# Kernel tuning notes

Measured on AMD Instinct MI355X. Metric: run time of the kernel, lower is better.

## Reference

```python
import jax, jax.numpy as jnp
import numpy as np

L = 8      # n_layers
D = 512    # msa_dim
P = 128    # pair_dim
H = 8      # n_heads
HD = D // H  # head_dim = 64
B = 2
NS = 4
S = 384


def setup_inputs() -> dict:
    key = jax.random.key(0)
    ks = jax.random.split(key, 24)
    def rn(k, shape, s=0.02):
        return jax.random.normal(k, shape, dtype=jnp.float32) * s
    return {
        "msa_repr": jax.random.normal(ks[0], (B, NS, S, D), dtype=jnp.float32),
        "pair_repr": jax.random.normal(ks[1], (B, S, S, P), dtype=jnp.float32),
        # per-layer IPA params, stacked along layer axis
        "Wq": rn(ks[2], (L, D, D)), "bq": jnp.zeros((L, D), jnp.float32),
        "Wk": rn(ks[3], (L, D, D)), "bk": jnp.zeros((L, D), jnp.float32),
        "Wv": rn(ks[4], (L, D, D)), "bv": jnp.zeros((L, D), jnp.float32),
        "Wpb": rn(ks[5], (L, P, H)), "bpb": jnp.zeros((L, H), jnp.float32),
        "Wo": rn(ks[6], (L, D, D)), "bo": jnp.zeros((L, D), jnp.float32),
        # shared backbone_update MLP (applied after every layer)
        "Wb1": rn(ks[7], (D, D)), "bb1": jnp.zeros((D,), jnp.float32),
        "Wb2": rn(ks[8], (D, 6)), "bb2": jnp.zeros((6,), jnp.float32),
        # confidence head
        "Wc1": rn(ks[9], (D, D // 2)), "bc1": jnp.zeros((D // 2,), jnp.float32),
        "Wc2": rn(ks[10], (D // 2, 1)), "bc2": jnp.zeros((1,), jnp.float32),
    }


def reference(msa_repr, pair_repr, Wq, bq, Wk, bk, Wv, bv, Wpb, bpb, Wo, bo,
              Wb1, bb1, Wb2, bb2, Wc1, bc1, Wc2, bc2):
    Bd, n_seqs, Sd, Dm = msa_repr.shape
    x0 = msa_repr[:, 0]                      # [B,S,D] target sequence repr
    coords0 = jnp.zeros((Bd, Sd, 3), msa_repr.dtype)
    inv_sqrt_hd = jnp.asarray(1.0 / np.sqrt(HD), msa_repr.dtype)

    def layer(carry, p):
        x, coords = carry
        wq, bq_, wk, bk_, wv, bv_, wpb, bpb_, wo, bo_ = p
        q = (x @ wq + bq_).reshape(Bd, Sd, H, HD)
        k = (x @ wk + bk_).reshape(Bd, Sd, H, HD)
        v = (x @ wv + bv_).reshape(Bd, Sd, H, HD)
        scores = jnp.einsum('bihd,bjhd->bhij', q, k) * inv_sqrt_hd
        bias = jnp.einsum('bijp,ph->bhij', pair_repr, wpb) + bpb_[None, :, None, None]
        attn = jax.nn.softmax(scores + bias, axis=-1)   # dropout=0 (eval)
        out = jnp.einsum('bhij,bjhd->bihd', attn, v).reshape(Bd, Sd, Dm)
        x = x + out @ wo + bo_                          # residual
        upd = jax.nn.relu(x @ Wb1 + bb1) @ Wb2 + bb2    # [B,S,6]
        coords = coords + upd[..., :3]                  # translation only
        return (x, coords), None

    (x, coords), _ = jax.lax.scan(layer, (x0, coords0),
                                  (Wq, bq, Wk, bk, Wv, bv, Wpb, bpb, Wo, bo))
    confidence = jax.nn.sigmoid(jax.nn.relu(x @ Wc1 + bc1) @ Wc2 + bc2)[..., 0]
    return coords, confidence
```

## Files before the change

### kernel.cpp

```cpp
#include <hip/hip_runtime.h>
#include <math.h>

#define L 8
#define D 512
#define DD (D*D)
#define P 128
#define H 8
#define HD 64
#define B 2
#define NS 4
#define S 384
#define BS (B*S)
#define XN (BS*D)
#define SS ((size_t)S*S)
#define BHSS ((size_t)B*H*S*S)
#define NSLAB 32

typedef short bf16x8 __attribute__((ext_vector_type(8)));
typedef float f32x4 __attribute__((ext_vector_type(4)));

__device__ __forceinline__ unsigned short f2b(float f) {
    unsigned u = __float_as_uint(f);
    unsigned r = (u + 0x7FFF + ((u >> 16) & 1)) >> 16;
    return (unsigned short)r;
}
__device__ __forceinline__ float b2f(unsigned short u) {
    return __uint_as_float(((unsigned)u) << 16);
}

__global__ __launch_bounds__(256) void k_init(const float* __restrict__ msa,
                                              float* __restrict__ x,
                                              unsigned short* __restrict__ xb,
                                              float* __restrict__ part) {
    int idx = blockIdx.x * 256 + threadIdx.x;
    if (idx < XN) {
        int b = idx / (S * D);
        int rem = idx - b * (S * D);
        float v = msa[(size_t)b * NS * S * D + rem];
        x[idx] = v;
        xb[idx] = f2b(v);
    }
    if (idx < NSLAB * BS * 3) part[idx] = 0.f;
}

__global__ __launch_bounds__(256) void k_prep(const float* __restrict__ Wq,
        const float* __restrict__ Wk, const float* __restrict__ Wv,
        const float* __restrict__ Wo, const float* __restrict__ Wb1,
        const float* __restrict__ Wc1, unsigned short* __restrict__ wt) {
    __shared__ float ts[64][65];
    const int z = blockIdx.z;
    const float* src; int N = 512;
    if (z < 8)       src = Wq + (size_t)z * DD;
    else if (z < 16) src = Wk + (size_t)(z - 8) * DD;
    else if (z < 24) src = Wv + (size_t)(z - 16) * DD;
    else if (z < 32) src = Wo + (size_t)(z - 24) * DD;
    else if (z == 32) src = Wb1;
    else { src = Wc1; N = 256; }
    unsigned short* dst = wt + (size_t)z * DD;

    const int n0 = blockIdx.x * 64, k0 = blockIdx.y * 64;
    if (n0 >= N) return;
    const int t = threadIdx.x;
    #pragma unroll
    for (int m = 0; m < 16; m++) {
        int f = t + m * 256;
        int r = f >> 6, c = f & 63;
        ts[r][c] = src[(size_t)(k0 + r) * N + n0 + c];
    }
    __syncthreads();
    #pragma unroll
    for (int m = 0; m < 4; m++) {
        int o4 = t + m * 256;
        int nr = o4 >> 4, k4 = o4 & 15;
        ushort4 pk;
        pk.x = f2b(ts[k4 * 4 + 0][nr]);
        pk.y = f2b(ts[k4 * 4 + 1][nr]);
        pk.z = f2b(ts[k4 * 4 + 2][nr]);
        pk.w = f2b(ts[k4 * 4 + 3][nr]);
        *(ushort4*)&dst[(size_t)(n0 + nr) * 512 + k0 + k4 * 4] = pk;
    }
}

__global__ __launch_bounds__(256) void k_biasm(const float* __restrict__ pair,
        const float* __restrict__ Wpb, const float* __restrict__ bpb,
        unsigned short* __restrict__ bias) {
    __shared__ unsigned short Ws[64][136];
    __shared__ unsigned short Ps[64][136];
    const int t = threadIdx.x;
    const int lane = t & 63, w = t >> 6;
    const int jt = blockIdx.x, i = blockIdx.y, b = blockIdx.z;

    #pragma unroll
    for (int m = 0; m < 8; m++) {
        int f = (t + m * 256) * 4;
        float4 wv = *(const float4*)&Wpb[f];
        int l = f >> 10, rem = f & 1023;
        int k = rem >> 3, h = rem & 7;
        int lh = (l << 3) | h;
        Ws[lh + 0][k] = f2b(wv.x);
        Ws[lh + 1][k] = f2b(wv.y);
        Ws[lh + 2][k] = f2b(wv.z);
        Ws[lh + 3][k] = f2b(wv.w);
    }
    const float* prow = pair + (((size_t)b * S + i) * S + jt * 64) * P;
    #pragma unroll
    for (int m = 0; m < 8; m++) {
        int f = (t + m * 256) * 4;
        int r = f >> 7, c = f & 127;
        float4 pv = *(const float4*)&prow[f];
        ushort4 u;
        u.x = f2b(pv.x); u.y = f2b(pv.y); u.z = f2b(pv.z); u.w = f2b(pv.w);
        *(ushort4*)&Ps[r][c] = u;
    }
    __syncthreads();

    f32x4 acc[4];
    #pragma unroll
    for (int mi = 0; mi < 4; mi++) { acc[mi][0] = 0.f; acc[mi][1] = 0.f; acc[mi][2] = 0.f; acc[mi][3] = 0.f; }
    #pragma unroll
    for (int ks = 0; ks < 4; ks++) {
        bf16x8 bv = *(const bf16x8*)&Ps[w * 16 + (lane & 15)][ks * 32 + (lane >> 4) * 8];
        #pragma unroll
        for (int mi = 0; mi < 4; mi++) {
            bf16x8 av = *(const bf16x8*)&Ws[mi * 16 + (lane & 15)][ks * 32 + (lane >> 4) * 8];
            acc[mi] = __builtin_amdgcn_mfma_f32_16x16x32_bf16(av, bv, acc[mi], 0, 0, 0);
        }
    }
    const int j = jt * 64 + w * 16 + (lane & 15);
    #pragma unroll
    for (int mi = 0; mi < 4; mi++)
        #pragma unroll
        for (int reg = 0; reg < 4; reg++) {
            int lh = mi * 16 + (lane >> 4) * 4 + reg;
            float v = acc[mi][reg] + bpb[lh];
            size_t plane = ((size_t)(lh >> 3) * B + b) * H + (lh & 7);
            bias[plane * SS + (size_t)i * S + j] = f2b(v);
        }
}

#define GEMM32_CORE(Abase, Wbase)                                              \
    f32x4 acc; acc[0] = 0.f; acc[1] = 0.f; acc[2] = 0.f; acc[3] = 0.f;         \
    {                                                                          \
        const unsigned short* pa = &(Abase)[(size_t)(m0 + sr) * 512 + scc];    \
        const unsigned short* pb = &(Wbase)[(size_t)(n0 + sr) * 512 + scc];    \
        int4 ra = *(const int4*)pa;                                            \
        int4 rb = *(const int4*)pb;                                            \
        for (int kt = 0; kt < 512; kt += 64) {                                 \
            *(int4*)&As[sr][scc] = ra;                                         \
            *(int4*)&Bs[sr][scc] = rb;                                         \
            __syncthreads();                                                   \
            if (kt + 64 < 512) {                                               \
                ra = *(const int4*)(pa + kt + 64);                             \
                rb = *(const int4*)(pb + kt + 64);                             \
            }                                                                  \
            _Pragma("unroll")                                                  \
            for (int kk = 0; kk < 2; kk++) {                                   \
                bf16x8 a = *(const bf16x8*)&As[wr * 16 + (lane & 15)][kk * 32 + (lane >> 4) * 8]; \
                bf16x8 bb = *(const bf16x8*)&Bs[wc * 16 + (lane & 15)][kk * 32 + (lane >> 4) * 8]; \
                acc = __builtin_amdgcn_mfma_f32_16x16x32_bf16(a, bb, acc, 0, 0, 0); \
            }                                                                  \
            __syncthreads();                                                   \
        }                                                                      \
    }

__global__ __launch_bounds__(256) void k_phaseA(const unsigned short* __restrict__ xb,
        const unsigned short* __restrict__ wt,
        const float* __restrict__ bq, const float* __restrict__ bk, const float* __restrict__ bv,
        unsigned short* __restrict__ qbb, unsigned short* __restrict__ kbb,
        unsigned short* __restrict__ vtb,
        const float* __restrict__ bb1, const float* __restrict__ Wb2g,
        float* __restrict__ part, int l) {
    __shared__ unsigned short As[32][72];
    __shared__ unsigned short Bs[32][72];
    const int t = threadIdx.x, lane = t & 63;
    const int w = t >> 6, wr = w >> 1, wc = w & 1;
    const int z = blockIdx.z;
    const int m0 = blockIdx.y * 32, n0 = blockIdx.x * 32;
    const int sr = t >> 3, scc = (t & 7) * 8;

    const unsigned short* Wt;
    const float* bias;
    if (z == 0)      { Wt = wt + (size_t)l * DD;        bias = bq + l * D; }
    else if (z == 1) { Wt = wt + (size_t)(8 + l) * DD;  bias = bk + l * D; }
    else if (z == 2) { Wt = wt + (size_t)(16 + l) * DD; bias = bv + l * D; }
    else             { Wt = wt + (size_t)32 * DD;       bias = bb1; }

    GEMM32_CORE(xb, Wt)

    const int col = n0 + wc * 16 + (lane & 15);
    const float bcol = bias[col];
    if (z < 3) {
        unsigned short* out = (z == 0) ? qbb : (z == 1) ? kbb : vtb;
        const int h = col >> 6, d = col & 63;
        #pragma unroll
        for (int reg = 0; reg < 4; reg++) {
            int row = m0 + wr * 16 + (lane >> 4) * 4 + reg;
            int b = row / S, i = row - b * S;
            float v = acc[reg] + bcol;
            if (z < 2) out[(((size_t)b * H + h) * S + i) * HD + d] = f2b(v);
            else       out[(((size_t)b * H + h) * HD + d) * S + i] = f2b(v);
        }
    } else {
        const float w20 = Wb2g[col * 6 + 0];
        const float w21 = Wb2g[col * 6 + 1];
        const float w22 = Wb2g[col * 6 + 2];
        #pragma unroll
        for (int reg = 0; reg < 4; reg++) {
            float v = fmaxf(acc[reg] + bcol, 0.f);
            float p0 = v * w20, p1 = v * w21, p2 = v * w22;
            #pragma unroll
            for (int m = 1; m < 16; m <<= 1) {
                p0 += __shfl_xor(p0, m);
                p1 += __shfl_xor(p1, m);
                p2 += __shfl_xor(p2, m);
            }
            if ((lane & 15) == 0) {
                int row = m0 + wr * 16 + (lane >> 4) * 4 + reg;
                float* pp = &part[((size_t)(blockIdx.x * 2 + wc) * BS + row) * 3];
                pp[0] += p0; pp[1] += p1; pp[2] += p2;
            }
        }
    }
}

__global__ __launch_bounds__(256) void k_wo(const unsigned short* __restrict__ aob,
        const unsigned short* __restrict__ wt, const float* __restrict__ bo,
        float* __restrict__ x, unsigned short* __restrict__ xb, int l) {
    __shared__ unsigned short As[32][72];
    __shared__ unsigned short Bs[32][72];
    const int t = threadIdx.x, lane = t & 63;
    const int w = t >> 6, wr = w >> 1, wc = w & 1;
    const int m0 = blockIdx.y * 32, n0 = blockIdx.x * 32;
    const int sr = t >> 3, scc = (t & 7) * 8;
    const unsigned short* Wt = wt + (size_t)(24 + l) * DD;

    GEMM32_CORE(aob, Wt)

    const int col = n0 + wc * 16 + (lane & 15);
    const float bcol = bo[l * D + col];
    #pragma unroll
    for (int reg = 0; reg < 4; reg++) {
        int row = m0 + wr * 16 + (lane >> 4) * 4 + reg;
        float v = acc[reg] + bcol + x[(size_t)row * D + col];
        x[(size_t)row * D + col] = v;
        xb[(size_t)row * D + col] = f2b(v);
    }
}

__global__ __launch_bounds__(256) void k_final(const unsigned short* __restrict__ xb,
        const unsigned short* __restrict__ wt,
        const float* __restrict__ bb1, const float* __restrict__ Wb2g, float* __restrict__ part,
        const float* __restrict__ bc1, float* __restrict__ hc) {
    __shared__ unsigned short As[32][72];
    __shared__ unsigned short Bs[32][72];
    const int t = threadIdx.x, lane = t & 63;
    const int w = t >> 6, wr = w >> 1, wc = w & 1;
    const int z = blockIdx.z;
    if (z == 1 && blockIdx.x >= 8) return;
    const int m0 = blockIdx.y * 32, n0 = blockIdx.x * 32;
    const int sr = t >> 3, scc = (t & 7) * 8;
    const unsigned short* Wt = (z == 0) ? wt + (size_t)32 * DD : wt + (size_t)33 * DD;

    GEMM32_CORE(xb, Wt)

    const int col = n0 + wc * 16 + (lane & 15);
    if (z == 0) {
        const float bcol = bb1[col];
        const float w20 = Wb2g[col * 6 + 0];
        const float w21 = Wb2g[col * 6 + 1];
        const float w22 = Wb2g[col * 6 + 2];
        #pragma unroll
        for (int reg = 0; reg < 4; reg++) {
            float v = fmaxf(acc[reg] + bcol, 0.f);
            float p0 = v * w20, p1 = v * w21, p2 = v * w22;
            #pragma unroll
            for (int m = 1; m < 16; m <<= 1) {
                p0 += __shfl_xor(p0, m);
                p1 += __shfl_xor(p1, m);
                p2 += __shfl_xor(p2, m);
            }
            if ((lane & 15) == 0) {
                int row = m0 + wr * 16 + (lane >> 4) * 4 + reg;
                float* pp = &part[((size_t)(blockIdx.x * 2 + wc) * BS + row) * 3];
                pp[0] += p0; pp[1] += p1; pp[2] += p2;
            }
        }
    } else {
        const float bcol = bc1[col];
        #pragma unroll
        for (int reg = 0; reg < 4; reg++) {
            int row = m0 + wr * 16 + (lane >> 4) * 4 + reg;
            hc[(size_t)row * 256 + col] = fmaxf(acc[reg] + bcol, 0.f);
        }
    }
}

__global__ __launch_bounds__(256) void k_attnm(const unsigned short* __restrict__ qb,
        const unsigned short* __restrict__ kb, const unsigned short* __restrict__ vt,
        const unsigned short* __restrict__ biasL, unsigned short* __restrict__ aob) {
    __shared__ unsigned short qs[16][72];
    __shared__ unsigned short kvsh[64][72];
    __shared__ float scs[16][392];
    __shared__ unsigned short pbs[16][392];
    __shared__ float invs[16];

    const int t = threadIdx.x, lane = t & 63, w = t >> 6;
    const int i0 = blockIdx.x * 16;
    const int h = blockIdx.y, b = blockIdx.z;
    const size_t bh = (size_t)b * H + h;
    const unsigned short* qp = qb + (bh * S + i0) * HD;
    const unsigned short* kp = kb + bh * S * HD;
    const unsigned short* vp = vt + bh * HD * S;
    const unsigned short* bp = biasL + bh * SS + (size_t)i0 * S;

    if (t < 128) {
        int r = t >> 3, c = (t & 7) * 8;
        *(int4*)&qs[r][c] = *(const int4*)&qp[r * HD + c];
    }
    #pragma unroll
    for (int m = 0; m < 3; m++) {
        int f = t + m * 256;
        int r = f / 48, c = (f % 48) * 8;
        *(int4*)&pbs[r][c] = *(const int4*)&bp[(size_t)r * S + c];
    }
    __syncthreads();

    bf16x8 qa0 = *(const bf16x8*)&qs[lane & 15][(lane >> 4) * 8];
    bf16x8 qa1 = *(const bf16x8*)&qs[lane & 15][32 + (lane >> 4) * 8];

    for (int jt = 0; jt < 6; jt++) {
        #pragma unroll
        for (int m = 0; m < 2; m++) {
            int g2 = t + m * 256;
            int r = g2 >> 3, c = (g2 & 7) * 8;
            *(int4*)&kvsh[r][c] = *(const int4*)&kp[(size_t)(jt * 64 + r) * HD + c];
        }
        __syncthreads();
        f32x4 acc; acc[0] = 0.f; acc[1] = 0.f; acc[2] = 0.f; acc[3] = 0.f;
        bf16x8 kb0 = *(const bf16x8*)&kvsh[w * 16 + (lane & 15)][(lane >> 4) * 8];
        bf16x8 kb1 = *(const bf16x8*)&kvsh[w * 16 + (lane & 15)][32 + (lane >> 4) * 8];
        acc = __builtin_amdgcn_mfma_f32_16x16x32_bf16(qa0, kb0, acc, 0, 0, 0);
        acc = __builtin_amdgcn_mfma_f32_16x16x32_bf16(qa1, kb1, acc, 0, 0, 0);
        const int col = jt * 64 + w * 16 + (lane & 15);
        #pragma unroll
        for (int reg = 0; reg < 4; reg++) {
            int row = (lane >> 4) * 4 + reg;
            scs[row][col] = acc[reg] * 0.125f + b2f(pbs[row][col]);
        }
        __syncthreads();
    }

    const int i = t >> 4, sub = t & 15;
    float mx = -1e30f;
    #pragma unroll
    for (int m = 0; m < 24; m++) mx = fmaxf(mx, scs[i][sub + m * 16]);
    #pragma unroll
    for (int m = 1; m < 16; m <<= 1) mx = fmaxf(mx, __shfl_xor(mx, m));
    float pv_[24];
    float sum = 0.f;
    #pragma unroll
    for (int m = 0; m < 24; m++) {
        float p = __expf(scs[i][sub + m * 16] - mx);
        pv_[m] = p;
        sum += p;
    }
    #pragma unroll
    for (int m = 1; m < 16; m <<= 1) sum += __shfl_xor(sum, m);
    if (sub == 0) invs[i] = 1.f / sum;
    __syncthreads();
    #pragma unroll
    for (int m = 0; m < 24; m++) pbs[i][sub + m * 16] = f2b(pv_[m]);
    __syncthreads();

    f32x4 oacc; oacc[0] = 0.f; oacc[1] = 0.f; oacc[2] = 0.f; oacc[3] = 0.f;
    for (int jt = 0; jt < 6; jt++) {
        #pragma unroll
        for (int m = 0; m < 2; m++) {
            int g2 = t + m * 256;
            int r = g2 >> 3, c = (g2 & 7) * 8;
            *(int4*)&kvsh[r][c] = *(const int4*)&vp[(size_t)r * S + jt * 64 + c];
        }
        __syncthreads();
        #pragma unroll
        for (int kk = 0; kk < 2; kk++) {
            bf16x8 pa = *(const bf16x8*)&pbs[lane & 15][jt * 64 + kk * 32 + (lane >> 4) * 8];
            bf16x8 bb = *(const bf16x8*)&kvsh[w * 16 + (lane & 15)][kk * 32 + (lane >> 4) * 8];
            oacc = __builtin_amdgcn_mfma_f32_16x16x32_bf16(pa, bb, oacc, 0, 0, 0);
        }
        __syncthreads();
    }
    #pragma unroll
    for (int reg = 0; reg < 4; reg++) {
        int row = (lane >> 4) * 4 + reg;
        int d = w * 16 + (lane & 15);
        float v = oacc[reg] * invs[row];
        aob[((size_t)(b * S + i0 + row)) * D + h * HD + d] = f2b(v);
    }
}

__global__ __launch_bounds__(256) void k_conf(const float* __restrict__ hc,
        const float* __restrict__ Wc2, const float* __restrict__ bc2,
        const float* __restrict__ part, const float* __restrict__ bb2,
        float* __restrict__ out) {
    const int wv = threadIdx.x >> 6, lane = threadIdx.x & 63;
    const int row = blockIdx.x * 4 + wv;
    const float* hr = hc + (size_t)row * 256;
    float p = 0.f;
    #pragma unroll
    for (int m = 0; m < 4; m++) p += hr[m * 64 + lane] * Wc2[m * 64 + lane];
    #pragma unroll
    for (int m = 32; m; m >>= 1) p += __shfl_xor(p, m);
    if (lane == 0) out[B * S * 3 + row] = 1.f / (1.f + __expf(-(p + bc2[0])));
    int ci = blockIdx.x * 12 + threadIdx.x;
    if (threadIdx.x < 12) {
        int r = ci / 3, c = ci - r * 3;
        float s = 8.f * bb2[c];
        #pragma unroll
        for (int nb = 0; nb < NSLAB; nb++) s += part[((size_t)nb * BS + r) * 3 + c];
        out[ci] = s;
    }
}

extern "C" void kernel_launch(void* const* d_in, const int* in_sizes, int n_in,
                              void* d_out, int out_size, void* d_ws, size_t ws_size,
                              hipStream_t stream) {
    const float* msa = (const float*)d_in[0];
    const float* pair = (const float*)d_in[1];
    const float* Wq = (const float*)d_in[2];
    const float* bq = (const float*)d_in[3];
    const float* Wk = (const float*)d_in[4];
    const float* bk = (const float*)d_in[5];
    const float* Wv = (const float*)d_in[6];
    const float* bv = (const float*)d_in[7];
    const float* Wpb = (const float*)d_in[8];
    const float* bpb = (const float*)d_in[9];
    const float* Wo = (const float*)d_in[10];
    const float* bo = (const float*)d_in[11];
    const float* Wb1 = (const float*)d_in[12];
    const float* bb1 = (const float*)d_in[13];
    const float* Wb2 = (const float*)d_in[14];
    const float* bb2 = (const float*)d_in[15];
    const float* Wc1 = (const float*)d_in[16];
    const float* bc1 = (const float*)d_in[17];
    const float* Wc2 = (const float*)d_in[18];
    const float* bc2 = (const float*)d_in[19];

    char* base = (char*)d_ws;
    float* x    = (float*)base;            base += (size_t)XN * 4;
    float* hc   = (float*)base;            base += (size_t)BS * 256 * 4;
    float* part = (float*)base;            base += (size_t)NSLAB * BS * 3 * 4;
    unsigned short* xb  = (unsigned short*)base;  base += (size_t)XN * 2;
    unsigned short* aob = (unsigned short*)base;  base += (size_t)XN * 2;
    unsigned short* qbb = (unsigned short*)base;  base += (size_t)XN * 2;
    unsigned short* kbb = (unsigned short*)base;  base += (size_t)XN * 2;
    unsigned short* vtb = (unsigned short*)base;  base += (size_t)XN * 2;
    unsigned short* wt  = (unsigned short*)base;  base += (size_t)34 * DD * 2;
    unsigned short* biasb = (unsigned short*)base;

    k_prep<<<dim3(8, 8, 34), 256, 0, stream>>>(Wq, Wk, Wv, Wo, Wb1, Wc1, wt);
    k_init<<<dim3(1536), 256, 0, stream>>>(msa, x, xb, part);
    k_biasm<<<dim3(6, S, B), 256, 0, stream>>>(pair, Wpb, bpb, biasb);

    for (int l = 0; l < L; ++l) {
        k_phaseA<<<dim3(16, 24, l == 0 ? 3 : 4), 256, 0, stream>>>(xb, wt,
            bq, bk, bv, qbb, kbb, vtb, bb1, Wb2, part, l);
        k_attnm<<<dim3(S / 16, H, B), 256, 0, stream>>>(qbb, kbb, vtb,
            biasb + (size_t)l * BHSS, aob);
        k_wo<<<dim3(16, 24), 256, 0, stream>>>(aob, wt, bo, x, xb, l);
    }

    k_final<<<dim3(16, 24, 2), 256, 0, stream>>>(xb, wt, bb1, Wb2, part, bc1, hc);
    k_conf<<<dim3(BS / 4), 256, 0, stream>>>(hc, Wc2, bc2, part, bb2, (float*)d_out);
}
```

Before: 267.6 us.

## Double-buffer shared memory tiles in GEMM core and attention kernel

Converts the shared-memory staging in the 32x32 GEMM macro and in the attention kernel's K/V loops to ping-pong double buffers. Each iteration now needs one barrier instead of two, and the next tile's global load overlaps with the MFMA work on the current tile. The attention kernel also prefetches the first V tile during the softmax and merges two barriers there. The cost is doubled LDS for these buffers, which may lower occupancy, plus extra registers held for the prefetched tiles.

Measured after the change: 252.7 us. 5.6% less time.

```diff
diff --git a/kernel.cpp b/kernel.cpp
--- a/kernel.cpp
+++ b/kernel.cpp
@@ -145,21 +145,27 @@
         const unsigned short* pb = &(Wbase)[(size_t)(n0 + sr) * 512 + scc];    \
         int4 ra = *(const int4*)pa;                                            \
         int4 rb = *(const int4*)pb;                                            \
+        *(int4*)&As[0][sr][scc] = ra;                                          \
+        *(int4*)&Bs[0][sr][scc] = rb;                                          \
+        __syncthreads();                                                       \
+        int cur = 0;                                                           \
         for (int kt = 0; kt < 512; kt += 64) {                                 \
-            *(int4*)&As[sr][scc] = ra;                                         \
-            *(int4*)&Bs[sr][scc] = rb;                                         \
-            __syncthreads();                                                   \
             if (kt + 64 < 512) {                                               \
                 ra = *(const int4*)(pa + kt + 64);                             \
                 rb = *(const int4*)(pb + kt + 64);                             \
             }                                                                  \
             _Pragma("unroll")                                                  \
             for (int kk = 0; kk < 2; kk++) {                                   \
-                bf16x8 a = *(const bf16x8*)&As[wr * 16 + (lane & 15)][kk * 32 + (lane >> 4) * 8]; \
-                bf16x8 bb = *(const bf16x8*)&Bs[wc * 16 + (lane & 15)][kk * 32 + (lane >> 4) * 8]; \
+                bf16x8 a = *(const bf16x8*)&As[cur][wr * 16 + (lane & 15)][kk * 32 + (lane >> 4) * 8]; \
+                bf16x8 bb = *(const bf16x8*)&Bs[cur][wc * 16 + (lane & 15)][kk * 32 + (lane >> 4) * 8]; \
                 acc = __builtin_amdgcn_mfma_f32_16x16x32_bf16(a, bb, acc, 0, 0, 0); \
             }                                                                  \
+            if (kt + 64 < 512) {                                               \
+                *(int4*)&As[cur ^ 1][sr][scc] = ra;                            \
+                *(int4*)&Bs[cur ^ 1][sr][scc] = rb;                            \
+            }                                                                  \
             __syncthreads();                                                   \
+            cur ^= 1;                                                          \
         }                                                                      \
     }
 
@@ -170,8 +176,8 @@
         unsigned short* __restrict__ vtb,
         const float* __restrict__ bb1, const float* __restrict__ Wb2g,
         float* __restrict__ part, int l) {
-    __shared__ unsigned short As[32][72];
-    __shared__ unsigned short Bs[32][72];
+    __shared__ unsigned short As[2][32][72];
+    __shared__ unsigned short Bs[2][32][72];
     const int t = threadIdx.x, lane = t & 63;
     const int w = t >> 6, wr = w >> 1, wc = w & 1;
     const int z = blockIdx.z;
@@ -226,8 +232,8 @@
 __global__ __launch_bounds__(256) void k_wo(const unsigned short* __restrict__ aob,
         const unsigned short* __restrict__ wt, const float* __restrict__ bo,
         float* __restrict__ x, unsigned short* __restrict__ xb, int l) {
-    __shared__ unsigned short As[32][72];
-    __shared__ unsigned short Bs[32][72];
+    __shared__ unsigned short As[2][32][72];
+    __shared__ unsigned short Bs[2][32][72];
     const int t = threadIdx.x, lane = t & 63;
     const int w = t >> 6, wr = w >> 1, wc = w & 1;
     const int m0 = blockIdx.y * 32, n0 = blockIdx.x * 32;
@@ -251,8 +257,8 @@
         const unsigned short* __restrict__ wt,
         const float* __restrict__ bb1, const float* __restrict__ Wb2g, float* __restrict__ part,
         const float* __restrict__ bc1, float* __restrict__ hc) {
-    __shared__ unsigned short As[32][72];
-    __shared__ unsigned short Bs[32][72];
+    __shared__ unsigned short As[2][32][72];
+    __shared__ unsigned short Bs[2][32][72];
     const int t = threadIdx.x, lane = t & 63;
     const int w = t >> 6, wr = w >> 1, wc = w & 1;
     const int z = blockIdx.z;
@@ -299,7 +305,7 @@
         const unsigned short* __restrict__ kb, const unsigned short* __restrict__ vt,
         const unsigned short* __restrict__ biasL, unsigned short* __restrict__ aob) {
     __shared__ unsigned short qs[16][72];
-    __shared__ unsigned short kvsh[64][72];
+    __shared__ unsigned short kv[2][64][72];
     __shared__ float scs[16][392];
     __shared__ unsigned short pbs[16][392];
     __shared__ float invs[16];
@@ -313,6 +319,8 @@
     const unsigned short* vp = vt + bh * HD * S;
     const unsigned short* bp = biasL + bh * SS + (size_t)i0 * S;
 
+    const int str = t >> 3, stc = (t & 7) * 8;
+
     if (t < 128) {
         int r = t >> 3, c = (t & 7) * 8;
         *(int4*)&qs[r][c] = *(const int4*)&qp[r * HD + c];
@@ -323,22 +331,23 @@
         int r = f / 48, c = (f % 48) * 8;
         *(int4*)&pbs[r][c] = *(const int4*)&bp[(size_t)r * S + c];
     }
+    *(int4*)&kv[0][str][stc]      = *(const int4*)&kp[(size_t)str * HD + stc];
+    *(int4*)&kv[0][32 + str][stc] = *(const int4*)&kp[(size_t)(32 + str) * HD + stc];
     __syncthreads();
 
     bf16x8 qa0 = *(const bf16x8*)&qs[lane & 15][(lane >> 4) * 8];
     bf16x8 qa1 = *(const bf16x8*)&qs[lane & 15][32 + (lane >> 4) * 8];
 
+    int cur = 0;
     for (int jt = 0; jt < 6; jt++) {
-        #pragma unroll
-        for (int m = 0; m < 2; m++) {
-            int g2 = t + m * 256;
-            int r = g2 >> 3, c = (g2 & 7) * 8;
-            *(int4*)&kvsh[r][c] = *(const int4*)&kp[(size_t)(jt * 64 + r) * HD + c];
-        }
-        __syncthreads();
+        int4 r0, r1;
+        if (jt < 5) {
+            r0 = *(const int4*)&kp[(size_t)((jt + 1) * 64 + str) * HD + stc];
+            r1 = *(const int4*)&kp[(size_t)((jt + 1) * 64 + 32 + str) * HD + stc];
+        }
         f32x4 acc; acc[0] = 0.f; acc[1] = 0.f; acc[2] = 0.f; acc[3] = 0.f;
-        bf16x8 kb0 = *(const bf16x8*)&kvsh[w * 16 + (lane & 15)][(lane >> 4) * 8];
-        bf16x8 kb1 = *(const bf16x8*)&kvsh[w * 16 + (lane & 15)][32 + (lane >> 4) * 8];
+        bf16x8 kb0 = *(const bf16x8*)&kv[cur][w * 16 + (lane & 15)][(lane >> 4) * 8];
+        bf16x8 kb1 = *(const bf16x8*)&kv[cur][w * 16 + (lane & 15)][32 + (lane >> 4) * 8];
         acc = __builtin_amdgcn_mfma_f32_16x16x32_bf16(qa0, kb0, acc, 0, 0, 0);
         acc = __builtin_amdgcn_mfma_f32_16x16x32_bf16(qa1, kb1, acc, 0, 0, 0);
         const int col = jt * 64 + w * 16 + (lane & 15);
@@ -347,9 +356,16 @@
             int row = (lane >> 4) * 4 + reg;
             scs[row][col] = acc[reg] * 0.125f + b2f(pbs[row][col]);
         }
+        if (jt < 5) {
+            *(int4*)&kv[cur ^ 1][str][stc]      = r0;
+            *(int4*)&kv[cur ^ 1][32 + str][stc] = r1;
+        }
         __syncthreads();
-    }
-
+        cur ^= 1;
+    }
+
+    int4 v0 = *(const int4*)&vp[(size_t)str * S + stc];
+    int4 v1 = *(const int4*)&vp[(size_t)(32 + str) * S + stc];
     const int i = t >> 4, sub = t & 15;
     float mx = -1e30f;
     #pragma unroll
@@ -367,27 +383,32 @@
     #pragma unroll
     for (int m = 1; m < 16; m <<= 1) sum += __shfl_xor(sum, m);
     if (sub == 0) invs[i] = 1.f / sum;
+    #pragma unroll
+    for (int m = 0; m < 24; m++) pbs[i][sub + m * 16] = f2b(pv_[m]);
+    *(int4*)&kv[0][str][stc]      = v0;
+    *(int4*)&kv[0][32 + str][stc] = v1;
     __syncthreads();
-    #pragma unroll
-    for (int m = 0; m < 24; m++) pbs[i][sub + m * 16] = f2b(pv_[m]);
-    __syncthreads();
 
     f32x4 oacc; oacc[0] = 0.f; oacc[1] = 0.f; oacc[2] = 0.f; oacc[3] = 0.f;
+    int vc = 0;
     for (int jt = 0; jt < 6; jt++) {
-        #pragma unroll
-        for (int m = 0; m < 2; m++) {
-            int g2 = t + m * 256;
-            int r = g2 >> 3, c = (g2 & 7) * 8;
-            *(int4*)&kvsh[r][c] = *(const int4*)&vp[(size_t)r * S + jt * 64 + c];
-        }
-        __syncthreads();
+        int4 w0, w1;
+        if (jt < 5) {
+            w0 = *(const int4*)&vp[(size_t)str * S + (jt + 1) * 64 + stc];
+            w1 = *(const int4*)&vp[(size_t)(32 + str) * S + (jt + 1) * 64 + stc];
+        }
         #pragma unroll
         for (int kk = 0; kk < 2; kk++) {
             bf16x8 pa = *(const bf16x8*)&pbs[lane & 15][jt * 64 + kk * 32 + (lane >> 4) * 8];
-            bf16x8 bb = *(const bf16x8*)&kvsh[w * 16 + (lane & 15)][kk * 32 + (lane >> 4) * 8];
+            bf16x8 bb = *(const bf16x8*)&kv[vc][w * 16 + (lane & 15)][kk * 32 + (lane >> 4) * 8];
             oacc = __builtin_amdgcn_mfma_f32_16x16x32_bf16(pa, bb, oacc, 0, 0, 0);
         }
+        if (jt < 5) {
+            *(int4*)&kv[vc ^ 1][str][stc]      = w0;
+            *(int4*)&kv[vc ^ 1][32 + str][stc] = w1;
+        }
         __syncthreads();
+        vc ^= 1;
     }
     #pragma unroll
     for (int reg = 0; reg < 4; reg++) {
```
